# Kernel tuning notes

Hardware: AMD Instinct MI355X
Metric: run time of the kernel (lower is better)

Reference implementation:

```python
import jax, jax.numpy as jnp
import numpy as np

# 8 corner offsets for neighborhood_size=1: lower and lower+1 in each dim
_OFFSETS = jnp.array([[dx, dy, dz] for dx in (0, 1) for dy in (0, 1) for dz in (0, 1)], dtype=jnp.int32)  # (8,3)


def setup_inputs() -> dict:
    key = jax.random.key(0)
    k1, k2 = jax.random.split(key)
    B, N, C, D = 4, 32768, 128, 32
    ptcloud = jax.random.uniform(k1, (B, N, 3), dtype=jnp.float32, minval=-1.0, maxval=1.0)
    cubic_features = jax.random.normal(k2, (B, C, D, D, D), dtype=jnp.float32)
    return {"ptcloud": ptcloud, "cubic_features": cubic_features}


def reference(ptcloud, cubic_features):
    # ptcloud: (B,N,3) in [-1,1]; cubic_features: (B,C,Dx,Dy,Dz)
    B, C, Dx, Dy, Dz = cubic_features.shape
    dims = jnp.array([Dx, Dy, Dz], dtype=jnp.int32)
    scaling = (jnp.array([Dx, Dy, Dz], dtype=jnp.float32) - 1.0) * 0.5
    p = (ptcloud + 1.0) * scaling  # (B,N,3) in voxel coords
    lower = jnp.floor(p).astype(jnp.int32)  # (B,N,3)
    idx = lower[:, :, None, :] + _OFFSETS[None, None, :, :]  # (B,N,8,3)
    valid = jnp.all((idx >= 0) & (idx < dims), axis=-1)  # (B,N,8)
    idx_c = jnp.clip(idx, 0, dims - 1)
    flat = (idx_c[..., 0] * Dy + idx_c[..., 1]) * Dz + idx_c[..., 2]  # (B,N,8)
    feats = cubic_features.reshape(B, C, Dx * Dy * Dz)  # (B,C,V)
    # gather: indices broadcast over channel axis -> (B,C,N*8)
    gathered = jnp.take_along_axis(feats, flat.reshape(B, 1, -1), axis=2)
    gathered = gathered.reshape(B, C, ptcloud.shape[1], 8).transpose(0, 2, 3, 1)  # (B,N,8,C)
    return gathered * valid[..., None].astype(gathered.dtype)
```

## Files before the change

kernel.cpp:

```cpp
#include <hip/hip_runtime.h>

#define B_ 4
#define N_ 32768
#define C_ 128
#define D_ 32
#define V_ (D_ * D_ * D_)

typedef float f4 __attribute__((ext_vector_type(4)));

__global__ __launch_bounds__(256) void transpose_kernel(
    const float* __restrict__ in,
    float* __restrict__ out)
{
    __shared__ float lds[C_ * 33];
    const int b  = blockIdx.y;
    const int v0 = blockIdx.x * 32;
    const float* inb  = in  + (size_t)b * C_ * V_;
    float*       outb = out + (size_t)b * C_ * V_;
    const int t = threadIdx.x;

    const int vq = t & 7;
    const int ci = t >> 3;
#pragma unroll
    for (int r = 0; r < 4; ++r) {
        const int c = ci + r * 32;
        const f4 f = __builtin_nontemporal_load(
            reinterpret_cast<const f4*>(inb + (size_t)c * V_ + v0 + vq * 4));
        float* d = &lds[c * 33 + vq * 4];
        d[0] = f.x; d[1] = f.y; d[2] = f.z; d[3] = f.w;
    }

    __syncthreads();

    const int c4 = (t & 31) << 2;
    const int vr = t >> 5;
#pragma unroll
    for (int r = 0; r < 4; ++r) {
        const int v = vr + r * 8;
        f4 g;
        g.x = lds[(c4 + 0) * 33 + v];
        g.y = lds[(c4 + 1) * 33 + v];
        g.z = lds[(c4 + 2) * 33 + v];
        g.w = lds[(c4 + 3) * 33 + v];
        *reinterpret_cast<f4*>(outb + (size_t)(v0 + v) * C_ + c4) = g;
    }
}

__global__ __launch_bounds__(256) void gather_kernel(
    const float* __restrict__ ptcloud,
    const float* __restrict__ featsT,
    float* __restrict__ out)
{
    const int t = threadIdx.x;
    const int point = (blockIdx.x << 2) + (t >> 6);
    const int l  = t & 63;
    const int kk = l >> 5;
    const int c4 = (l & 31) << 2;
    const int b  = point >> 15;

    const float* pp = ptcloud + (size_t)point * 3;
    const float s = (D_ - 1) * 0.5f;
    const float fx = (pp[0] + 1.0f) * s;
    const float fy = (pp[1] + 1.0f) * s;
    const float fz = (pp[2] + 1.0f) * s;
    const int lx = (int)floorf(fx);
    const int ly = (int)floorf(fy);
    const int lz = (int)floorf(fz);

    const int iz = lz + kk;
    const bool vz = (unsigned)iz < (unsigned)D_;
    const int cz = min(max(iz, 0), D_ - 1);

    const float* src = featsT + (size_t)b * V_ * C_ + c4;
    float* dst = out + ((size_t)point * 8 + kk) * C_ + c4;

    f4 v[4];
    float m[4];
#pragma unroll
    for (int j = 0; j < 4; ++j) {
        const int ix = lx + (j >> 1);
        const int iy = ly + (j & 1);
        const bool valid = vz &
                           ((unsigned)ix < (unsigned)D_) &
                           ((unsigned)iy < (unsigned)D_);
        const int cx = min(max(ix, 0), D_ - 1);
        const int cy = min(max(iy, 0), D_ - 1);
        const int flat = (cx * D_ + cy) * D_ + cz;
        v[j] = *reinterpret_cast<const f4*>(src + (size_t)flat * C_);
        m[j] = valid ? 1.0f : 0.0f;
    }

#pragma unroll
    for (int j = 0; j < 4; ++j) {
        f4 r = v[j] * m[j];
        __builtin_nontemporal_store(
            r, reinterpret_cast<f4*>(dst + (size_t)(2 * j) * C_));
    }
}

__global__ __launch_bounds__(128) void gather_direct_kernel(
    const float* __restrict__ ptcloud,
    const float* __restrict__ feats,
    float* __restrict__ out)
{
    const int point = blockIdx.x;
    const int b = point >> 15;
    const int c = threadIdx.x;

    const float* pp = ptcloud + (size_t)point * 3;
    const float s = (D_ - 1) * 0.5f;
    const int lx = (int)floorf((pp[0] + 1.0f) * s);
    const int ly = (int)floorf((pp[1] + 1.0f) * s);
    const int lz = (int)floorf((pp[2] + 1.0f) * s);

    const float* fb = feats + ((size_t)b * C_ + c) * V_;
    float* ob = out + (size_t)point * 8 * C_ + c;

#pragma unroll
    for (int k = 0; k < 8; ++k) {
        const int ix = lx + (k >> 2);
        const int iy = ly + ((k >> 1) & 1);
        const int iz = lz + (k & 1);
        const bool valid = ((unsigned)ix < (unsigned)D_) &
                           ((unsigned)iy < (unsigned)D_) &
                           ((unsigned)iz < (unsigned)D_);
        const int cx = min(max(ix, 0), D_ - 1);
        const int cy = min(max(iy, 0), D_ - 1);
        const int cz = min(max(iz, 0), D_ - 1);
        const int flat = (cx * D_ + cy) * D_ + cz;
        ob[(size_t)k * C_] = fb[flat] * (valid ? 1.0f : 0.0f);
    }
}

extern "C" void kernel_launch(void* const* d_in, const int* in_sizes, int n_in,
                              void* d_out, int out_size, void* d_ws, size_t ws_size,
                              hipStream_t stream) {
    const float* ptcloud = (const float*)d_in[0];
    const float* feats   = (const float*)d_in[1];
    float* out = (float*)d_out;

    const size_t need = (size_t)B_ * C_ * V_ * sizeof(float);
    if (ws_size >= need) {
        float* featsT = (float*)d_ws;
        dim3 tg(V_ / 32, B_);
        transpose_kernel<<<tg, 256, 0, stream>>>(feats, featsT);
        gather_kernel<<<(B_ * N_) / 4, 256, 0, stream>>>(ptcloud, featsT, out);
    } else {
        gather_direct_kernel<<<B_ * N_, 128, 0, stream>>>(ptcloud, feats, out);
    }
}
```

Measured before the change: 607.4 us.

## Bucket-sort points by voxel block before gathering to improve cache locality

Adds a counting sort over points, bucketed by 4x4x4 voxel blocks per batch: zero histogram, atomic histogram, single-block scan, and atomic scatter into an order array. The gather kernel then processes points in sorted order, so neighbouring blocks read nearby voxel rows of the transposed features and get more cache reuse. This costs four extra small launches, atomics, and a scattered output write pattern, because each point still writes to its original location. It also needs a larger workspace; if the workspace is too small, the code falls back to the unsorted path.

```diff
diff --git a/kernel.cpp b/kernel.cpp
--- a/kernel.cpp
+++ b/kernel.cpp
@@ -5,6 +5,8 @@
 #define C_ 128
 #define D_ 32
 #define V_ (D_ * D_ * D_)
+#define NBUCK 512
+#define NBUCK_T (NBUCK * B_)
 
 typedef float f4 __attribute__((ext_vector_type(4)));
 
@@ -46,13 +48,66 @@
     }
 }
 
+__device__ __forceinline__ int bucket_of(const float* __restrict__ pp) {
+    const float s = (D_ - 1) * 0.5f;
+    const int lx = (int)floorf((pp[0] + 1.0f) * s);
+    const int ly = (int)floorf((pp[1] + 1.0f) * s);
+    const int lz = (int)floorf((pp[2] + 1.0f) * s);
+    return ((lx >> 2) << 6) | ((ly >> 2) << 3) | (lz >> 2);
+}
+
+__global__ __launch_bounds__(256) void zero_hist_kernel(unsigned* __restrict__ hist) {
+    hist[blockIdx.x * 256 + threadIdx.x] = 0u;
+}
+
+__global__ __launch_bounds__(256) void hist_kernel(
+    const float* __restrict__ ptcloud, unsigned* __restrict__ hist)
+{
+    const int p = blockIdx.x * 256 + threadIdx.x;
+    const int bg = ((p >> 15) << 9) | bucket_of(ptcloud + (size_t)p * 3);
+    atomicAdd(&hist[bg], 1u);
+}
+
+__global__ __launch_bounds__(256) void scan_kernel(
+    const unsigned* __restrict__ hist, unsigned* __restrict__ cursor)
+{
+    __shared__ unsigned ssum[256];
+    const int t = threadIdx.x;
+    unsigned v[8], s = 0;
+#pragma unroll
+    for (int i = 0; i < 8; ++i) { v[i] = hist[t * 8 + i]; s += v[i]; }
+    ssum[t] = s;
+    __syncthreads();
+    for (int ofs = 1; ofs < 256; ofs <<= 1) {
+        const unsigned x = (t >= ofs) ? ssum[t - ofs] : 0u;
+        __syncthreads();
+        ssum[t] += x;
+        __syncthreads();
+    }
+    unsigned run = ssum[t] - s;
+#pragma unroll
+    for (int i = 0; i < 8; ++i) { cursor[t * 8 + i] = run; run += v[i]; }
+}
+
+__global__ __launch_bounds__(256) void scatter_kernel(
+    const float* __restrict__ ptcloud, unsigned* __restrict__ cursor,
+    unsigned* __restrict__ order)
+{
+    const int p = blockIdx.x * 256 + threadIdx.x;
+    const int bg = ((p >> 15) << 9) | bucket_of(ptcloud + (size_t)p * 3);
+    const unsigned pos = atomicAdd(&cursor[bg], 1u);
+    order[pos] = (unsigned)p;
+}
+
 __global__ __launch_bounds__(256) void gather_kernel(
     const float* __restrict__ ptcloud,
     const float* __restrict__ featsT,
-    float* __restrict__ out)
-{
-    const int t = threadIdx.x;
-    const int point = (blockIdx.x << 2) + (t >> 6);
+    const unsigned* __restrict__ order,
+    float* __restrict__ out)
+{
+    const int t = threadIdx.x;
+    const int sp = (blockIdx.x << 2) + (t >> 6);
+    const int point = (int)order[sp];
     const int l  = t & 63;
     const int kk = l >> 5;
     const int c4 = (l & 31) << 2;
@@ -60,12 +115,9 @@
 
     const float* pp = ptcloud + (size_t)point * 3;
     const float s = (D_ - 1) * 0.5f;
-    const float fx = (pp[0] + 1.0f) * s;
-    const float fy = (pp[1] + 1.0f) * s;
-    const float fz = (pp[2] + 1.0f) * s;
-    const int lx = (int)floorf(fx);
-    const int ly = (int)floorf(fy);
-    const int lz = (int)floorf(fz);
+    const int lx = (int)floorf((pp[0] + 1.0f) * s);
+    const int ly = (int)floorf((pp[1] + 1.0f) * s);
+    const int lz = (int)floorf((pp[2] + 1.0f) * s);
 
     const int iz = lz + kk;
     const bool vz = (unsigned)iz < (unsigned)D_;
@@ -90,6 +142,54 @@
         m[j] = valid ? 1.0f : 0.0f;
     }
 
+#pragma unroll
+    for (int j = 0; j < 4; ++j) {
+        f4 r = v[j] * m[j];
+        __builtin_nontemporal_store(
+            r, reinterpret_cast<f4*>(dst + (size_t)(2 * j) * C_));
+    }
+}
+
+__global__ __launch_bounds__(256) void gather_unsorted_kernel(
+    const float* __restrict__ ptcloud,
+    const float* __restrict__ featsT,
+    float* __restrict__ out)
+{
+    const int t = threadIdx.x;
+    const int point = (blockIdx.x << 2) + (t >> 6);
+    const int l  = t & 63;
+    const int kk = l >> 5;
+    const int c4 = (l & 31) << 2;
+    const int b  = point >> 15;
+
+    const float* pp = ptcloud + (size_t)point * 3;
+    const float s = (D_ - 1) * 0.5f;
+    const int lx = (int)floorf((pp[0] + 1.0f) * s);
+    const int ly = (int)floorf((pp[1] + 1.0f) * s);
+    const int lz = (int)floorf((pp[2] + 1.0f) * s);
+
+    const int iz = lz + kk;
+    const bool vz = (unsigned)iz < (unsigned)D_;
+    const int cz = min(max(iz, 0), D_ - 1);
+
+    const float* src = featsT + (size_t)b * V_ * C_ + c4;
+    float* dst = out + ((size_t)point * 8 + kk) * C_ + c4;
+
+    f4 v[4];
+    float m[4];
+#pragma unroll
+    for (int j = 0; j < 4; ++j) {
+        const int ix = lx + (j >> 1);
+        const int iy = ly + (j & 1);
+        const bool valid = vz &
+                           ((unsigned)ix < (unsigned)D_) &
+                           ((unsigned)iy < (unsigned)D_);
+        const int cx = min(max(ix, 0), D_ - 1);
+        const int cy = min(max(iy, 0), D_ - 1);
+        const int flat = (cx * D_ + cy) * D_ + cz;
+        v[j] = *reinterpret_cast<const f4*>(src + (size_t)flat * C_);
+        m[j] = valid ? 1.0f : 0.0f;
+    }
 #pragma unroll
     for (int j = 0; j < 4; ++j) {
         f4 r = v[j] * m[j];
@@ -139,12 +239,30 @@
     const float* feats   = (const float*)d_in[1];
     float* out = (float*)d_out;
 
-    const size_t need = (size_t)B_ * C_ * V_ * sizeof(float);
-    if (ws_size >= need) {
+    const size_t featsT_bytes = (size_t)B_ * C_ * V_ * sizeof(float);
+    const size_t hist_bytes   = NBUCK_T * sizeof(unsigned);
+    const size_t order_bytes  = (size_t)B_ * N_ * sizeof(unsigned);
+    const size_t need_sort    = featsT_bytes + 2 * hist_bytes + order_bytes;
+
+    if (ws_size >= need_sort) {
+        char* w = (char*)d_ws;
+        float*    featsT = (float*)w;
+        unsigned* hist   = (unsigned*)(w + featsT_bytes);
+        unsigned* cursor = (unsigned*)(w + featsT_bytes + hist_bytes);
+        unsigned* order  = (unsigned*)(w + featsT_bytes + 2 * hist_bytes);
+
+        dim3 tg(V_ / 32, B_);
+        transpose_kernel<<<tg, 256, 0, stream>>>(feats, featsT);
+        zero_hist_kernel<<<NBUCK_T / 256, 256, 0, stream>>>(hist);
+        hist_kernel<<<(B_ * N_) / 256, 256, 0, stream>>>(ptcloud, hist);
+        scan_kernel<<<1, 256, 0, stream>>>(hist, cursor);
+        scatter_kernel<<<(B_ * N_) / 256, 256, 0, stream>>>(ptcloud, cursor, order);
+        gather_kernel<<<(B_ * N_) / 4, 256, 0, stream>>>(ptcloud, featsT, order, out);
+    } else if (ws_size >= featsT_bytes) {
         float* featsT = (float*)d_ws;
         dim3 tg(V_ / 32, B_);
         transpose_kernel<<<tg, 256, 0, stream>>>(feats, featsT);
-        gather_kernel<<<(B_ * N_) / 4, 256, 0, stream>>>(ptcloud, featsT, out);
+        gather_unsorted_kernel<<<(B_ * N_) / 4, 256, 0, stream>>>(ptcloud, featsT, out);
     } else {
         gather_direct_kernel<<<B_ * N_, 128, 0, stream>>>(ptcloud, feats, out);
     }
```

Result: slower. 643.4 us (+5.9%).
